# Kernel optimization log

Hardware: AMD Instinct MI355X
Metric: run time of the kernel (lower is better)

## Reference

```python
import jax, jax.numpy as jnp
import numpy as np

# Model dims (Llama-7B-like GQA)
S, B, D_MODEL = 2048, 2, 4096   # total seq, batch, hidden
NH, NKV, HD = 32, 8, 128        # q heads, kv heads, head dim
TP = 4                          # ring size -> number of KV blocks
SB = S // TP                    # KV block length per ring step


def setup_inputs() -> dict:
    key = jax.random.key(0)
    k1, k2, k3 = jax.random.split(key, 3)
    hidden_states = jax.random.normal(k1, (S, B, D_MODEL), jnp.float32)
    w_qkv = jax.random.normal(k2, (D_MODEL, (NH + 2 * NKV) * HD), jnp.float32) / np.sqrt(D_MODEL)
    w_o = jax.random.normal(k3, (NH * HD, D_MODEL), jnp.float32) / np.sqrt(NH * HD)
    return {"hidden_states": hidden_states, "w_qkv": w_qkv, "w_o": w_o}


def _ring_attention(hidden_states, w_qkv, w_o):
    # fused QKV projection: [S,B,D] @ [D,(NH+2*NKV)*HD]
    qkv = hidden_states @ w_qkv
    q, k, v = jnp.split(qkv, [NH * HD, (NH + NKV) * HD], axis=-1)
    q = q.reshape(S, B, NH, HD).transpose(1, 2, 0, 3)    # [B,NH,S,HD]
    k = k.reshape(S, B, NKV, HD).transpose(1, 2, 0, 3)   # [B,NKV,S,HD]
    v = v.reshape(S, B, NKV, HD).transpose(1, 2, 0, 3)

    groups = NH // NKV  # GQA: expand kv heads to match q heads
    k = jnp.repeat(k, groups, axis=1)  # [B,NH,S,HD]
    v = jnp.repeat(v, groups, axis=1)

    scale = 1.0 / np.sqrt(HD)

    # Split K/V along sequence into TP ring blocks: [TP,B,NH,SB,HD]
    k_blocks = k.reshape(B, NH, TP, SB, HD).transpose(2, 0, 1, 3, 4)
    v_blocks = v.reshape(B, NH, TP, SB, HD).transpose(2, 0, 1, 3, 4)

    # Online-softmax (flash-attention style) accumulation over ring steps.
    m0 = jnp.full((B, NH, S), -jnp.inf, q.dtype)   # running row max
    l0 = jnp.zeros((B, NH, S), q.dtype)            # running denom
    acc0 = jnp.zeros((B, NH, S, HD), q.dtype)      # running numerator

    def step(carry, kv):
        m, l, acc = carry
        kb, vb = kv  # [B,NH,SB,HD]
        s = jnp.einsum('bhqd,bhkd->bhqk', q, kb) * scale  # [B,NH,S,SB]
        m_new = jnp.maximum(m, s.max(-1))
        p = jnp.exp(s - m_new[..., None])
        alpha = jnp.exp(m - m_new)
        l = l * alpha + p.sum(-1)
        acc = acc * alpha[..., None] + jnp.einsum('bhqk,bhkd->bhqd', p, vb)
        return (m_new, l, acc), None

    (m, l, acc), _ = jax.lax.scan(step, (m0, l0, acc0), (k_blocks, v_blocks))
    attn = acc / l[..., None]  # [B,NH,S,HD]

    # [B,NH,S,HD] -> [S*B, NH*HD] -> o_proj -> [S,B,D]
    attn = attn.transpose(2, 0, 1, 3).reshape(S * B, NH * HD)
    return (attn @ w_o).reshape(S, B, D_MODEL)


def reference(hidden_states, w_qkv, w_o):
    return _ring_attention(hidden_states, w_qkv, w_o)
```

## Files before the change

### kernel.cpp

```cpp
#include <hip/hip_runtime.h>
#include <hip/hip_bf16.h>


typedef __bf16 bf16x8 __attribute__((ext_vector_type(8)));
typedef float f32x4 __attribute__((ext_vector_type(4)));
typedef unsigned short u16;
typedef u16 u16x4 __attribute__((ext_vector_type(4)));
typedef u16 u16x8 __attribute__((ext_vector_type(8)));
typedef unsigned int u32;

#define SEQ    2048
#define BATCH  2
#define NROWS  4096
#define DM     4096
#define QKVC   6144
#define QSCALE (0.08838834764831845f * 1.4426950408889634f)

__device__ __forceinline__ u16 f2bf(float f) {
  union { float f; u32 u; } v; v.f = f;
  u32 r = v.u + 0x7fffu + ((v.u >> 16) & 1u);
  return (u16)(r >> 16);
}

__device__ __forceinline__ void gload16(const void* g, void* l) {
  __builtin_amdgcn_global_load_lds(
      (const __attribute__((address_space(1))) unsigned int*)g,
      (__attribute__((address_space(3))) unsigned int*)l, 16, 0, 0);
}

__global__ __launch_bounds__(256) void conv_f32_bf16(
    const float* __restrict__ in, u16* __restrict__ out) {
  size_t i = ((size_t)blockIdx.x * 256 + threadIdx.x) * 8;
  float4 a = *(const float4*)(in + i);
  float4 b = *(const float4*)(in + i + 4);
  u16x8 o;
  o[0] = f2bf(a.x); o[1] = f2bf(a.y); o[2] = f2bf(a.z); o[3] = f2bf(a.w);
  o[4] = f2bf(b.x); o[5] = f2bf(b.y); o[6] = f2bf(b.z); o[7] = f2bf(b.w);
  *(u16x8*)(out + i) = o;
}

__global__ __launch_bounds__(256) void transpose_f32_bf16(
    const float* __restrict__ in, u16* __restrict__ out, int K, int N) {
  __shared__ u16 tile[64][65];
  const int k0 = blockIdx.y * 64, n0 = blockIdx.x * 64;
  const int t = threadIdx.x;
#pragma unroll
  for (int i = 0; i < 4; ++i) {
    int slot = i * 256 + t;
    int r = slot >> 4, cq = slot & 15;
    float4 v = *(const float4*)(in + (size_t)(k0 + r) * N + n0 + cq * 4);
    tile[cq * 4 + 0][r] = f2bf(v.x);
    tile[cq * 4 + 1][r] = f2bf(v.y);
    tile[cq * 4 + 2][r] = f2bf(v.z);
    tile[cq * 4 + 3][r] = f2bf(v.w);
  }
  __syncthreads();
#pragma unroll
  for (int i = 0; i < 2; ++i) {
    int slot = i * 256 + t;
    int n = slot >> 3, q = slot & 7;
    u16x8 o;
#pragma unroll
    for (int e = 0; e < 8; ++e) o[e] = tile[n][q * 8 + e];
    *(u16x8*)(out + (size_t)(n0 + n) * K + k0 + q * 8) = o;
  }
}

__global__ __launch_bounds__(256) void vtrans(
    const u16* __restrict__ qkv, u16* __restrict__ vt) {
  __shared__ u16 tile[64][66];
  const int s0 = blockIdx.x * 64, d0 = blockIdx.y * 64;
  const int z = blockIdx.z;
  const int b = z >> 3, kvh = z & 7;
  const int t = threadIdx.x;
#pragma unroll
  for (int i = 0; i < 2; ++i) {
    int chunk = i * 256 + t;
    int r = chunk >> 3, q = chunk & 7;
    u16x8 v = *(const u16x8*)&qkv[(size_t)((s0 + r) * 2 + b) * QKVC + 5120 + kvh * 128 + d0 + q * 8];
#pragma unroll
    for (int e = 0; e < 8; ++e) tile[r][q * 8 + e] = v[e];
  }
  __syncthreads();
#pragma unroll
  for (int i = 0; i < 2; ++i) {
    int chunk = i * 256 + t;
    int d = chunk >> 3, q = chunk & 7;
    u16x8 o;
#pragma unroll
    for (int e = 0; e < 8; ++e) o[e] = tile[q * 8 + e][d];
    *(u16x8*)&vt[(size_t)(z * 128 + d0 + d) * SEQ + s0 + q * 8] = o;
  }
}

template <int CBF16, int SCALEQ>
__global__ __launch_bounds__(512, 4) void gemm128(
    const u16* __restrict__ A, const u16* __restrict__ B,
    void* __restrict__ C, int M, int N, int K, int nby) {
  __shared__ u16 As[2 * 8192];
  __shared__ u16 Bs[2 * 12288];
  const int t = threadIdx.x;
  const int w = t >> 6, l = t & 63;
  const int g = l >> 4, c = l & 15;
  const int wm = w >> 2, wn = w & 3;

  const int nwg = gridDim.x;
  const int sid = (blockIdx.x & 7) * (nwg >> 3) + (blockIdx.x >> 3);
  const int by = sid % nby, bx = sid / nby;
  const int m0 = by * 128, n0 = bx * 192;

  const int gsrc = (l & 7) ^ (l >> 3);
  const u16* pA = A + (size_t)(m0 + w * 8 + (l >> 3)) * K + gsrc * 8;
  const u16* pB = B + (size_t)(n0 + w * 8 + (l >> 3)) * K + gsrc * 8;

#define STG128(tt) do { int d_ = (tt) & 1;                                  \
    _Pragma("unroll")                                                       \
    for (int u = 0; u < 2; ++u)                                             \
      gload16(pA + (size_t)(u * 64) * K + (size_t)(tt) * 64,                \
              &As[d_ * 8192 + u * 4096 + w * 512]);                         \
    _Pragma("unroll")                                                       \
    for (int u = 0; u < 3; ++u)                                             \
      gload16(pB + (size_t)(u * 64) * K + (size_t)(tt) * 64,                \
              &Bs[d_ * 12288 + u * 4096 + w * 512]); } while (0)

  const int xr0 = ((0 + g) ^ (c & 7)) << 3;
  const int xr1 = ((4 + g) ^ (c & 7)) << 3;

  const f32x4 fz = {0.f, 0.f, 0.f, 0.f};
  f32x4 acc[4][3];
#pragma unroll
  for (int m = 0; m < 4; ++m)
#pragma unroll
    for (int n = 0; n < 3; ++n) acc[m][n] = fz;

  const int nkt = K >> 6;
  STG128(0);
  for (int tt = 0; tt < nkt; ++tt) {
    const int d = tt & 1;
    if (tt + 1 < nkt) {
      STG128(tt + 1);
      asm volatile("s_waitcnt vmcnt(5)" ::: "memory");
    } else {
      asm volatile("s_waitcnt vmcnt(0)" ::: "memory");
    }
    __builtin_amdgcn_sched_barrier(0);
    __builtin_amdgcn_s_barrier();

    const u16* aT = &As[d * 8192 + (wm * 64 + c) * 64];
    const u16* bT = &Bs[d * 12288 + (wn * 48 + c) * 64];
    bf16x8 av[4][2], bv[3][2];
#pragma unroll
    for (int m = 0; m < 4; ++m) {
      av[m][0] = *(const bf16x8*)(aT + m * 1024 + xr0);
      av[m][1] = *(const bf16x8*)(aT + m * 1024 + xr1);
    }
#pragma unroll
    for (int n = 0; n < 3; ++n) {
      bv[n][0] = *(const bf16x8*)(bT + n * 1024 + xr0);
      bv[n][1] = *(const bf16x8*)(bT + n * 1024 + xr1);
    }
    __builtin_amdgcn_s_setprio(1);
#pragma unroll
    for (int kk = 0; kk < 2; ++kk)
#pragma unroll
      for (int m = 0; m < 4; ++m)
#pragma unroll
        for (int n = 0; n < 3; ++n)
          acc[m][n] = __builtin_amdgcn_mfma_f32_16x16x32_bf16(
              av[m][kk], bv[n][kk], acc[m][n], 0, 0, 0);
    __builtin_amdgcn_s_setprio(0);
    __builtin_amdgcn_s_barrier();
  }
#undef STG128

#pragma unroll
  for (int m = 0; m < 4; ++m)
#pragma unroll
    for (int n = 0; n < 3; ++n) {
      int row = m0 + wm * 64 + m * 16 + g * 4;
      int col = n0 + wn * 48 + n * 16 + c;
      float sc = (SCALEQ && col < 4096) ? QSCALE : 1.0f;
#pragma unroll
      for (int r = 0; r < 4; ++r) {
        float x = acc[m][n][r] * sc;
        if (CBF16) ((u16*)C)[(size_t)(row + r) * N + col] = f2bf(x);
        else       ((float*)C)[(size_t)(row + r) * N + col] = x;
      }
    }
}

template <int CBF16, int SCALEQ>
__global__ __launch_bounds__(512, 2) void gemm256(
    const u16* __restrict__ A, const u16* __restrict__ B,
    void* __restrict__ C, int M, int N, int K, int nby) {
  __shared__ u16 As[2 * 2 * 8192];
  __shared__ u16 Bs[2 * 2 * 8192];
  const int t = threadIdx.x;
  const int w = t >> 6, l = t & 63;
  const int g = l >> 4, c = l & 15;
  const int wm = w >> 2, wn = w & 3;

  const int nwg = gridDim.x;
  const int sid = (blockIdx.x & 7) * (nwg >> 3) + (blockIdx.x >> 3);
  const int by = sid % nby, bx = sid / nby;
  const int m0 = by * 256, n0 = bx * 256;

  const int gsrc = (l & 7) ^ (l >> 3);
  const u16* pA = A + (size_t)(m0 + w * 8 + (l >> 3)) * K + gsrc * 8;
  const u16* pB = B + (size_t)(n0 + w * 8 + (l >> 3)) * K + gsrc * 8;

#define STG_A(h, tt) do { int d_ = (tt) & 1;                                    \
    gload16(pA + (size_t)((h) * 128) * K + (tt) * 64,                           \
            &As[(d_ * 2 + (h)) * 8192 + w * 512]);                              \
    gload16(pA + (size_t)((h) * 128 + 64) * K + (tt) * 64,                      \
            &As[(d_ * 2 + (h)) * 8192 + 4096 + w * 512]); } while (0)
#define STG_B(h, tt) do { int d_ = (tt) & 1;                                    \
    gload16(pB + (size_t)((h) * 128) * K + (tt) * 64,                           \
            &Bs[(d_ * 2 + (h)) * 8192 + w * 512]);                              \
    gload16(pB + (size_t)((h) * 128 + 64) * K + (tt) * 64,                      \
            &Bs[(d_ * 2 + (h)) * 8192 + 4096 + w * 512]); } while (0)

  const u16* aRd = &As[wm * 8192 + c * 64];
  const u16* bRd = &Bs[(wn >> 1) * 8192 + ((wn & 1) * 64 + c) * 64];
  const int xr0 = ((0 + g) ^ (c & 7)) << 3;
  const int xr1 = ((4 + g) ^ (c & 7)) << 3;

  const f32x4 fz = {0.f, 0.f, 0.f, 0.f};
  f32x4 acc[8][4];
#pragma unroll
  for (int mi = 0; mi < 8; ++mi)
#pragma unroll
    for (int nj = 0; nj < 4; ++nj) acc[mi][nj] = fz;

  const int nkt = K >> 6;
  STG_A(0, 0); STG_A(1, 0); STG_B(0, 0); STG_B(1, 0);
  STG_B(0, 1); STG_B(1, 1);
  asm volatile("s_waitcnt vmcnt(4)" ::: "memory");
  __builtin_amdgcn_sched_barrier(0);
  __builtin_amdgcn_s_barrier();

  for (int tt = 0; tt < nkt; ++tt) {
    const int d = tt & 1;
    const u16* aT = aRd + d * 16384;
    const u16* bT = bRd + d * 16384;
    bf16x8 av[4][2], b01[2][2], b23[2][2];

#pragma unroll
    for (int m = 0; m < 4; ++m) {
      av[m][0] = *(const bf16x8*)(aT + m * 1024 + xr0);
      av[m][1] = *(const bf16x8*)(aT + m * 1024 + xr1);
    }
#pragma unroll
    for (int n = 0; n < 2; ++n) {
      b01[n][0] = *(const bf16x8*)(bT + n * 1024 + xr0);
      b01[n][1] = *(const bf16x8*)(bT + n * 1024 + xr1);
    }
    if (tt + 1 < nkt) STG_A(0, tt + 1);
    __builtin_amdgcn_s_barrier();
    __builtin_amdgcn_s_setprio(1);
#pragma unroll
    for (int kk = 0; kk < 2; ++kk)
#pragma unroll
      for (int m = 0; m < 4; ++m)
#pragma unroll
        for (int n = 0; n < 2; ++n)
          acc[m][n] = __builtin_amdgcn_mfma_f32_16x16x32_bf16(
              av[m][kk], b01[n][kk], acc[m][n], 0, 0, 0);
    __builtin_amdgcn_s_setprio(0);
    __builtin_amdgcn_s_barrier();

#pragma unroll
    for (int n = 0; n < 2; ++n) {
      b23[n][0] = *(const bf16x8*)(bT + (2 + n) * 1024 + xr0);
      b23[n][1] = *(const bf16x8*)(bT + (2 + n) * 1024 + xr1);
    }
    if (tt + 1 < nkt) STG_A(1, tt + 1);
    __builtin_amdgcn_s_barrier();
    __builtin_amdgcn_s_setprio(1);
#pragma unroll
    for (int kk = 0; kk < 2; ++kk)
#pragma unroll
      for (int m = 0; m < 4; ++m)
#pragma unroll
        for (int n = 0; n < 2; ++n)
          acc[m][2 + n] = __builtin_amdgcn_mfma_f32_16x16x32_bf16(
              av[m][kk], b23[n][kk], acc[m][2 + n], 0, 0, 0);
    __builtin_amdgcn_s_setprio(0);
    __builtin_amdgcn_s_barrier();

#pragma unroll
    for (int m = 0; m < 4; ++m) {
      av[m][0] = *(const bf16x8*)(aT + (4 + m) * 1024 + xr0);
      av[m][1] = *(const bf16x8*)(aT + (4 + m) * 1024 + xr1);
    }
    if (tt + 2 < nkt) STG_B(0, tt + 2);
    __builtin_amdgcn_s_barrier();
    __builtin_amdgcn_s_setprio(1);
#pragma unroll
    for (int kk = 0; kk < 2; ++kk)
#pragma unroll
      for (int m = 0; m < 4; ++m)
#pragma unroll
        for (int n = 0; n < 2; ++n)
          acc[4 + m][2 + n] = __builtin_amdgcn_mfma_f32_16x16x32_bf16(
              av[m][kk], b23[n][kk], acc[4 + m][2 + n], 0, 0, 0);
    __builtin_amdgcn_s_setprio(0);
    __builtin_amdgcn_s_barrier();

    if (tt + 2 < nkt) STG_B(1, tt + 2);
    if (tt < nkt - 2) asm volatile("s_waitcnt vmcnt(4)" ::: "memory");
    else              asm volatile("s_waitcnt vmcnt(0)" ::: "memory");
    __builtin_amdgcn_sched_barrier(0);
    __builtin_amdgcn_s_barrier();
    __builtin_amdgcn_s_setprio(1);
#pragma unroll
    for (int kk = 0; kk < 2; ++kk)
#pragma unroll
      for (int m = 0; m < 4; ++m)
#pragma unroll
        for (int n = 0; n < 2; ++n)
          acc[4 + m][n] = __builtin_amdgcn_mfma_f32_16x16x32_bf16(
              av[m][kk], b01[n][kk], acc[4 + m][n], 0, 0, 0);
    __builtin_amdgcn_s_setprio(0);
    __builtin_amdgcn_s_barrier();
  }
#undef STG_A
#undef STG_B

#pragma unroll
  for (int mi = 0; mi < 8; ++mi)
#pragma unroll
    for (int nj = 0; nj < 4; ++nj) {
      int row = m0 + wm * 128 + mi * 16 + g * 4;
      int col = n0 + wn * 64 + nj * 16 + c;
      float sc = (SCALEQ && col < 4096) ? QSCALE : 1.0f;
#pragma unroll
      for (int r = 0; r < 4; ++r) {
        float x = acc[mi][nj][r] * sc;
        if (CBF16) ((u16*)C)[(size_t)(row + r) * N + col] = f2bf(x);
        else       ((float*)C)[(size_t)(row + r) * N + col] = x;
      }
    }
}

__global__ __launch_bounds__(512, 4) void attn_fwd2(
    const u16* __restrict__ qkv, const u16* __restrict__ vtg,
    u16* __restrict__ out) {
  __shared__ u16 Ks[2][64 * 128];
  __shared__ u16 Vs[2][128 * 64];
  __shared__ u16 Ps[8][16 * 64];
  const int t = threadIdx.x;
  const int w = t >> 6, lane = t & 63;
  const int g = lane >> 4, c = lane & 15;
  const int bh = blockIdx.y;
  const int b = bh >> 5, h = bh & 31, kvh = h >> 2;
  const int q0 = blockIdx.x * 128 + w * 16;

  bf16x8 qf[4];
#pragma unroll
  for (int kk = 0; kk < 4; ++kk)
    qf[kk] = *(const bf16x8*)&qkv[(size_t)((q0 + c) * 2 + b) * QKVC + h * 128 + kk * 32 + g * 8];

  const f32x4 fz = {0.f, 0.f, 0.f, 0.f};
  f32x4 acc[8];
#pragma unroll
  for (int db = 0; db < 8; ++db) acc[db] = fz;
  float m_ = -__builtin_inff(), l_ = 0.f;

  const int w4g = w * 4 + g;
  const u16* pK = qkv + (size_t)b * QKVC + 4096 + kvh * 128 + (size_t)((c ^ w4g) & 15) * 8;
  const int vrow = w * 8 + (lane >> 3);
  const u16* pV = vtg + (size_t)(b * 8 + kvh) * 128 * SEQ + (size_t)((lane & 7) ^ (lane >> 3)) * 8;

  auto stage = [&](int bufi, int kv0) {
#pragma unroll
    for (int j = 0; j < 2; ++j)
      gload16(pK + (size_t)(kv0 + j * 32 + w4g) * (2 * QKVC), &Ks[bufi][(j * 8 + w) * 512]);
#pragma unroll
    for (int j = 0; j < 2; ++j)
      gload16(pV + (size_t)(j * 64 + vrow) * SEQ + kv0, &Vs[bufi][(j * 8 + w) * 512]);
  };

  stage(0, 0);
  int buf = 0;
  for (int kv0 = 0; kv0 < SEQ; kv0 += 64) {
    __syncthreads();
    if (kv0 + 64 < SEQ) stage(buf ^ 1, kv0 + 64);

    f32x4 st[4];
    __builtin_amdgcn_s_setprio(1);
#pragma unroll
    for (int kf = 0; kf < 4; ++kf) {
      const u16* kr = &Ks[buf][(kf * 16 + c) * 128];
      bf16x8 kfr[4];
#pragma unroll
      for (int kk = 0; kk < 4; ++kk)
        kfr[kk] = *(const bf16x8*)&kr[(((kk * 4 + g) ^ c) & 15) * 8];
      f32x4 s = fz;
#pragma unroll
      for (int kk = 0; kk < 4; ++kk)
        s = __builtin_amdgcn_mfma_f32_16x16x32_bf16(kfr[kk], qf[kk], s, 0, 0, 0);
      st[kf] = s;
    }
    __builtin_amdgcn_s_setprio(0);

    float mloc = st[0][0];
#pragma unroll
    for (int kf = 0; kf < 4; ++kf)
#pragma unroll
      for (int r = 0; r < 4; ++r) mloc = fmaxf(mloc, st[kf][r]);
    mloc = fmaxf(mloc, __shfl_xor(mloc, 16));
    mloc = fmaxf(mloc, __shfl_xor(mloc, 32));
    if (!__all(mloc - m_ <= 8.0f)) {
      float mnew = fmaxf(m_, mloc);
      float alpha = __builtin_amdgcn_exp2f(m_ - mnew);
      l_ *= alpha;
      f32x4 av;
#pragma unroll
      for (int r = 0; r < 4; ++r) av[r] = __shfl(alpha, g * 4 + r);
#pragma unroll
      for (int db = 0; db < 8; ++db) acc[db] *= av;
      m_ = mnew;
    }
    float ps = 0.f;
#pragma unroll
    for (int kf = 0; kf < 4; ++kf) {
      u16x4 pk;
#pragma unroll
      for (int r = 0; r < 4; ++r) {
        float p = __builtin_amdgcn_exp2f(st[kf][r] - m_);
        ps += p;
        pk[r] = f2bf(p);
      }
      *(u16x4*)&Ps[w][c * 64 + ((((kf * 2 + (g >> 1)) ^ (c & 7)) << 3) | ((g & 1) << 2))] = pk;
    }
    ps += __shfl_xor(ps, 16);
    ps += __shfl_xor(ps, 32);
    l_ += ps;

    bf16x8 pa0 = *(const bf16x8*)&Ps[w][c * 64 + (((0 + g) ^ (c & 7)) << 3)];
    bf16x8 pa1 = *(const bf16x8*)&Ps[w][c * 64 + (((4 + g) ^ (c & 7)) << 3)];
    __builtin_amdgcn_s_setprio(1);
#pragma unroll
    for (int db = 0; db < 8; ++db) {
      const u16* vr = &Vs[buf][(db * 16 + c) * 64];
      bf16x8 v0 = *(const bf16x8*)&vr[(((0 + g) ^ (c & 7)) << 3)];
      bf16x8 v1 = *(const bf16x8*)&vr[(((4 + g) ^ (c & 7)) << 3)];
      acc[db] = __builtin_amdgcn_mfma_f32_16x16x32_bf16(pa0, v0, acc[db], 0, 0, 0);
      acc[db] = __builtin_amdgcn_mfma_f32_16x16x32_bf16(pa1, v1, acc[db], 0, 0, 0);
    }
    __builtin_amdgcn_s_setprio(0);
    buf ^= 1;
  }

  float linv = __builtin_amdgcn_rcpf(l_);
  f32x4 il;
#pragma unroll
  for (int r = 0; r < 4; ++r) il[r] = __shfl(linv, g * 4 + r);
#pragma unroll
  for (int db = 0; db < 8; ++db) {
#pragma unroll
    for (int r = 0; r < 4; ++r) {
      int s = q0 + g * 4 + r;
      out[(size_t)(s * 2 + b) * DM + h * 128 + db * 16 + c] = f2bf(acc[db][r] * il[r]);
    }
  }
}

extern "C" void kernel_launch(void* const* d_in, const int* in_sizes, int n_in,
                              void* d_out, int out_size, void* d_ws, size_t ws_size,
                              hipStream_t stream) {
  const float* hidden = (const float*)d_in[0];
  const float* w_qkv  = (const float*)d_in[1];
  const float* w_o    = (const float*)d_in[2];
  float* outp = (float*)d_out;

  const size_t SZ_X  = (size_t)NROWS * DM * 2;
  const size_t SZ_WQ = (size_t)QKVC * DM * 2;
  const size_t SZ_WO = (size_t)DM * DM * 2;
  const size_t SZ_QKV = (size_t)NROWS * QKVC * 2;
  if (ws_size < SZ_X + SZ_WQ + SZ_WO + SZ_QKV) return;

  char* ws = (char*)d_ws;
  u16* Xb    = (u16*)ws;
  u16* WqkvT = (u16*)(ws + SZ_X);
  u16* WoT   = (u16*)(ws + SZ_X + SZ_WQ);
  u16* QKVb  = (u16*)(ws + SZ_X + SZ_WQ + SZ_WO);
  u16* VtG   = WqkvT;
  u16* Attn  = Xb;

  conv_f32_bf16<<<(NROWS * (size_t)DM) / 2048, 256, 0, stream>>>(hidden, Xb);
  transpose_f32_bf16<<<dim3(QKVC / 64, DM / 64), 256, 0, stream>>>(w_qkv, WqkvT, DM, QKVC);
  transpose_f32_bf16<<<dim3(DM / 64, DM / 64), 256, 0, stream>>>(w_o, WoT, DM, DM);
  gemm128<1, 1><<<1024, 512, 0, stream>>>(Xb, WqkvT, QKVb, NROWS, QKVC, DM, 32);
  vtrans<<<dim3(SEQ / 64, 2, 16), 256, 0, stream>>>(QKVb, VtG);
  attn_fwd2<<<dim3(SEQ / 128, BATCH * 32), 512, 0, stream>>>(QKVb, VtG, Attn);
  gemm256<0, 0><<<256, 512, 0, stream>>>(Attn, WoT, outp, NROWS, DM, DM, 16);
}
```

Before: 532.7 us.

## Give each attention wave two 16-row query tiles to reuse K/V fragments

The attention kernel now launches 256 threads (4 waves) per block instead of 512, and each wave handles 32 query rows as two 16-row sub-tiles. Each K and V fragment read from LDS feeds two MFMAs, halving LDS fragment traffic per unit of compute. Staging loops double per thread to cover the same 64-key tile. The cost is more registers per wave (two accumulator sets, two Q sets) and fewer waves to hide latency, which may reduce occupancy.

```diff
diff --git a/kernel.cpp b/kernel.cpp
--- a/kernel.cpp
+++ b/kernel.cpp
@@ -343,42 +343,47 @@
     }
 }
 
-__global__ __launch_bounds__(512, 4) void attn_fwd2(
+__global__ __launch_bounds__(256, 2) void attn_fwd3(
     const u16* __restrict__ qkv, const u16* __restrict__ vtg,
     u16* __restrict__ out) {
   __shared__ u16 Ks[2][64 * 128];
   __shared__ u16 Vs[2][128 * 64];
-  __shared__ u16 Ps[8][16 * 64];
+  __shared__ u16 Ps[4][32 * 64];
   const int t = threadIdx.x;
   const int w = t >> 6, lane = t & 63;
   const int g = lane >> 4, c = lane & 15;
   const int bh = blockIdx.y;
   const int b = bh >> 5, h = bh & 31, kvh = h >> 2;
-  const int q0 = blockIdx.x * 128 + w * 16;
-
-  bf16x8 qf[4];
-#pragma unroll
-  for (int kk = 0; kk < 4; ++kk)
-    qf[kk] = *(const bf16x8*)&qkv[(size_t)((q0 + c) * 2 + b) * QKVC + h * 128 + kk * 32 + g * 8];
+  const int q0 = blockIdx.x * 128 + w * 32;
+
+  bf16x8 qf[2][4];
+#pragma unroll
+  for (int qb = 0; qb < 2; ++qb)
+#pragma unroll
+    for (int kk = 0; kk < 4; ++kk)
+      qf[qb][kk] = *(const bf16x8*)&qkv[(size_t)((q0 + qb * 16 + c) * 2 + b) * QKVC + h * 128 + kk * 32 + g * 8];
 
   const f32x4 fz = {0.f, 0.f, 0.f, 0.f};
-  f32x4 acc[8];
-#pragma unroll
-  for (int db = 0; db < 8; ++db) acc[db] = fz;
-  float m_ = -__builtin_inff(), l_ = 0.f;
+  f32x4 acc[2][8];
+#pragma unroll
+  for (int qb = 0; qb < 2; ++qb)
+#pragma unroll
+    for (int db = 0; db < 8; ++db) acc[qb][db] = fz;
+  float m_[2] = {-__builtin_inff(), -__builtin_inff()};
+  float l_[2] = {0.f, 0.f};
 
   const int w4g = w * 4 + g;
   const u16* pK = qkv + (size_t)b * QKVC + 4096 + kvh * 128 + (size_t)((c ^ w4g) & 15) * 8;
   const int vrow = w * 8 + (lane >> 3);
-  const u16* pV = vtg + (size_t)(b * 8 + kvh) * 128 * SEQ + (size_t)((lane & 7) ^ (lane >> 3)) * 8;
+  const u16* pV = vtg + (size_t)(b * 8 + kvh) * 128 * SEQ + (size_t)((lane & 7) ^ ((lane >> 3) & 7)) * 8;
 
   auto stage = [&](int bufi, int kv0) {
 #pragma unroll
-    for (int j = 0; j < 2; ++j)
-      gload16(pK + (size_t)(kv0 + j * 32 + w4g) * (2 * QKVC), &Ks[bufi][(j * 8 + w) * 512]);
-#pragma unroll
-    for (int j = 0; j < 2; ++j)
-      gload16(pV + (size_t)(j * 64 + vrow) * SEQ + kv0, &Vs[bufi][(j * 8 + w) * 512]);
+    for (int j = 0; j < 4; ++j)
+      gload16(pK + (size_t)(kv0 + j * 16 + w4g) * (2 * QKVC), &Ks[bufi][(j * 4 + w) * 512]);
+#pragma unroll
+    for (int j = 0; j < 4; ++j)
+      gload16(pV + (size_t)(j * 32 + vrow) * SEQ + kv0, &Vs[bufi][(j * 4 + w) * 512]);
   };
 
   stage(0, 0);
@@ -387,7 +392,7 @@
     __syncthreads();
     if (kv0 + 64 < SEQ) stage(buf ^ 1, kv0 + 64);
 
-    f32x4 st[4];
+    f32x4 st[2][4];
     __builtin_amdgcn_s_setprio(1);
 #pragma unroll
     for (int kf = 0; kf < 4; ++kf) {
@@ -396,73 +401,91 @@
 #pragma unroll
       for (int kk = 0; kk < 4; ++kk)
         kfr[kk] = *(const bf16x8*)&kr[(((kk * 4 + g) ^ c) & 15) * 8];
-      f32x4 s = fz;
-#pragma unroll
-      for (int kk = 0; kk < 4; ++kk)
-        s = __builtin_amdgcn_mfma_f32_16x16x32_bf16(kfr[kk], qf[kk], s, 0, 0, 0);
-      st[kf] = s;
-    }
-    __builtin_amdgcn_s_setprio(0);
-
-    float mloc = st[0][0];
-#pragma unroll
-    for (int kf = 0; kf < 4; ++kf)
-#pragma unroll
-      for (int r = 0; r < 4; ++r) mloc = fmaxf(mloc, st[kf][r]);
-    mloc = fmaxf(mloc, __shfl_xor(mloc, 16));
-    mloc = fmaxf(mloc, __shfl_xor(mloc, 32));
-    if (!__all(mloc - m_ <= 8.0f)) {
-      float mnew = fmaxf(m_, mloc);
-      float alpha = __builtin_amdgcn_exp2f(m_ - mnew);
-      l_ *= alpha;
-      f32x4 av;
-#pragma unroll
-      for (int r = 0; r < 4; ++r) av[r] = __shfl(alpha, g * 4 + r);
-#pragma unroll
-      for (int db = 0; db < 8; ++db) acc[db] *= av;
-      m_ = mnew;
-    }
-    float ps = 0.f;
-#pragma unroll
-    for (int kf = 0; kf < 4; ++kf) {
-      u16x4 pk;
-#pragma unroll
-      for (int r = 0; r < 4; ++r) {
-        float p = __builtin_amdgcn_exp2f(st[kf][r] - m_);
-        ps += p;
-        pk[r] = f2bf(p);
-      }
-      *(u16x4*)&Ps[w][c * 64 + ((((kf * 2 + (g >> 1)) ^ (c & 7)) << 3) | ((g & 1) << 2))] = pk;
-    }
-    ps += __shfl_xor(ps, 16);
-    ps += __shfl_xor(ps, 32);
-    l_ += ps;
-
-    bf16x8 pa0 = *(const bf16x8*)&Ps[w][c * 64 + (((0 + g) ^ (c & 7)) << 3)];
-    bf16x8 pa1 = *(const bf16x8*)&Ps[w][c * 64 + (((4 + g) ^ (c & 7)) << 3)];
+#pragma unroll
+      for (int qb = 0; qb < 2; ++qb) {
+        f32x4 s = fz;
+#pragma unroll
+        for (int kk = 0; kk < 4; ++kk)
+          s = __builtin_amdgcn_mfma_f32_16x16x32_bf16(kfr[kk], qf[qb][kk], s, 0, 0, 0);
+        st[qb][kf] = s;
+      }
+    }
+    __builtin_amdgcn_s_setprio(0);
+
+#pragma unroll
+    for (int qb = 0; qb < 2; ++qb) {
+      float mloc = st[qb][0][0];
+#pragma unroll
+      for (int kf = 0; kf < 4; ++kf)
+#pragma unroll
+        for (int r = 0; r < 4; ++r) mloc = fmaxf(mloc, st[qb][kf][r]);
+      mloc = fmaxf(mloc, __shfl_xor(mloc, 16));
+      mloc = fmaxf(mloc, __shfl_xor(mloc, 32));
+      if (!__all(mloc - m_[qb] <= 8.0f)) {
+        float mnew = fmaxf(m_[qb], mloc);
+        float alpha = __builtin_amdgcn_exp2f(m_[qb] - mnew);
+        l_[qb] *= alpha;
+        f32x4 av;
+#pragma unroll
+        for (int r = 0; r < 4; ++r) av[r] = __shfl(alpha, g * 4 + r);
+#pragma unroll
+        for (int db = 0; db < 8; ++db) acc[qb][db] *= av;
+        m_[qb] = mnew;
+      }
+      float ps = 0.f;
+#pragma unroll
+      for (int kf = 0; kf < 4; ++kf) {
+        u16x4 pk;
+#pragma unroll
+        for (int r = 0; r < 4; ++r) {
+          float p = __builtin_amdgcn_exp2f(st[qb][kf][r] - m_[qb]);
+          ps += p;
+          pk[r] = f2bf(p);
+        }
+        int prow = qb * 16 + c;
+        *(u16x4*)&Ps[w][prow * 64 + ((((kf * 2 + (g >> 1)) ^ (c & 7)) << 3) | ((g & 1) << 2))] = pk;
+      }
+      ps += __shfl_xor(ps, 16);
+      ps += __shfl_xor(ps, 32);
+      l_[qb] += ps;
+    }
+
+    bf16x8 pa[2][2];
+#pragma unroll
+    for (int qb = 0; qb < 2; ++qb) {
+      int prow = qb * 16 + c;
+      pa[qb][0] = *(const bf16x8*)&Ps[w][prow * 64 + (((0 + g) ^ (c & 7)) << 3)];
+      pa[qb][1] = *(const bf16x8*)&Ps[w][prow * 64 + (((4 + g) ^ (c & 7)) << 3)];
+    }
     __builtin_amdgcn_s_setprio(1);
 #pragma unroll
     for (int db = 0; db < 8; ++db) {
       const u16* vr = &Vs[buf][(db * 16 + c) * 64];
       bf16x8 v0 = *(const bf16x8*)&vr[(((0 + g) ^ (c & 7)) << 3)];
       bf16x8 v1 = *(const bf16x8*)&vr[(((4 + g) ^ (c & 7)) << 3)];
-      acc[db] = __builtin_amdgcn_mfma_f32_16x16x32_bf16(pa0, v0, acc[db], 0, 0, 0);
-      acc[db] = __builtin_amdgcn_mfma_f32_16x16x32_bf16(pa1, v1, acc[db], 0, 0, 0);
+#pragma unroll
+      for (int qb = 0; qb < 2; ++qb) {
+        acc[qb][db] = __builtin_amdgcn_mfma_f32_16x16x32_bf16(pa[qb][0], v0, acc[qb][db], 0, 0, 0);
+        acc[qb][db] = __builtin_amdgcn_mfma_f32_16x16x32_bf16(pa[qb][1], v1, acc[qb][db], 0, 0, 0);
+      }
     }
     __builtin_amdgcn_s_setprio(0);
     buf ^= 1;
   }
 
-  float linv = __builtin_amdgcn_rcpf(l_);
-  f32x4 il;
-#pragma unroll
-  for (int r = 0; r < 4; ++r) il[r] = __shfl(linv, g * 4 + r);
-#pragma unroll
-  for (int db = 0; db < 8; ++db) {
-#pragma unroll
-    for (int r = 0; r < 4; ++r) {
-      int s = q0 + g * 4 + r;
-      out[(size_t)(s * 2 + b) * DM + h * 128 + db * 16 + c] = f2bf(acc[db][r] * il[r]);
+#pragma unroll
+  for (int qb = 0; qb < 2; ++qb) {
+    float linv = __builtin_amdgcn_rcpf(l_[qb]);
+    f32x4 il;
+#pragma unroll
+    for (int r = 0; r < 4; ++r) il[r] = __shfl(linv, g * 4 + r);
+#pragma unroll
+    for (int db = 0; db < 8; ++db) {
+#pragma unroll
+      for (int r = 0; r < 4; ++r) {
+        int s = q0 + qb * 16 + g * 4 + r;
+        out[(size_t)(s * 2 + b) * DM + h * 128 + db * 16 + c] = f2bf(acc[qb][db][r] * il[r]);
+      }
     }
   }
 }
@@ -494,6 +517,6 @@
   transpose_f32_bf16<<<dim3(DM / 64, DM / 64), 256, 0, stream>>>(w_o, WoT, DM, DM);
   gemm128<1, 1><<<1024, 512, 0, stream>>>(Xb, WqkvT, QKVb, NROWS, QKVC, DM, 32);
   vtrans<<<dim3(SEQ / 64, 2, 16), 256, 0, stream>>>(QKVb, VtG);
-  attn_fwd2<<<dim3(SEQ / 128, BATCH * 32), 512, 0, stream>>>(QKVb, VtG, Attn);
+  attn_fwd3<<<dim3(SEQ / 128, BATCH * 32), 256, 0, stream>>>(QKVb, VtG, Attn);
   gemm256<0, 0><<<256, 512, 0, stream>>>(Attn, WoT, outp, NROWS, DM, DM, 16);
 }
```

After: 535.2 us. About the same (+0.5%).
